# Kernel tuning notes

Hardware: AMD Instinct MI355X
Metric: run time of the kernel (lower is better)

Reference implementation:

```python
import jax, jax.numpy as jnp
import numpy as np

N_NODES = 50000
N_EDGES = 800000
NODE_DIM = 256
EDGE_DIM = 64
NUM_REL = 4
HID = 512      # hidden_dims[0]
LAST = 128     # last_dim_size
BATCH = 16384
EPS = 1e-10    # torchdrug RelationalGraphConv degree-normalization eps


def _glorot(k, shape):
    fan_in = shape[-1]
    return jax.random.normal(k, shape, jnp.float32) / np.sqrt(fan_in).astype(np.float32)


def setup_inputs() -> dict:
    key = jax.random.key(0)
    ks = jax.random.split(key, 20)
    inp = {}
    inp["inputs"] = jax.random.randint(ks[0], (BATCH, 3), 0, N_NODES, dtype=jnp.int32)
    inp["node_feature"] = jax.random.normal(ks[1], (N_NODES, NODE_DIM), jnp.float32)
    inp["edge_feature"] = jax.random.normal(ks[2], (N_EDGES, EDGE_DIM), jnp.float32)
    inp["edge_src"] = jax.random.randint(ks[3], (N_EDGES,), 0, N_NODES, dtype=jnp.int32)
    inp["edge_dst"] = jax.random.randint(ks[4], (N_EDGES,), 0, N_NODES, dtype=jnp.int32)
    inp["edge_rel"] = jax.random.randint(ks[5], (N_EDGES,), 0, NUM_REL, dtype=jnp.int32)
    # RGCN layer 1: 256 -> 512
    inp["We1"] = _glorot(ks[6], (NODE_DIM, EDGE_DIM)); inp["be1"] = jnp.zeros((NODE_DIM,), jnp.float32)
    inp["Wl1"] = _glorot(ks[7], (HID, NUM_REL * NODE_DIM)); inp["bl1"] = jnp.zeros((HID,), jnp.float32)
    inp["Ws1"] = _glorot(ks[8], (HID, NODE_DIM)); inp["bs1"] = jnp.zeros((HID,), jnp.float32)
    # RGCN layer 2: 512 -> 128
    inp["We2"] = _glorot(ks[9], (HID, EDGE_DIM)); inp["be2"] = jnp.zeros((HID,), jnp.float32)
    inp["Wl2"] = _glorot(ks[10], (LAST, NUM_REL * HID)); inp["bl2"] = jnp.zeros((LAST,), jnp.float32)
    inp["Ws2"] = _glorot(ks[11], (LAST, HID)); inp["bs2"] = jnp.zeros((LAST,), jnp.float32)
    # ccle_mlp: edge_dim -> 256 -> 128
    inp["Wc1"] = _glorot(ks[12], (256, EDGE_DIM)); inp["bc1"] = jnp.zeros((256,), jnp.float32)
    inp["Wc2"] = _glorot(ks[13], (LAST, 256)); inp["bc2"] = jnp.zeros((LAST,), jnp.float32)
    # final MLP: 3*128 -> 128 -> 64 -> 1
    inp["Wf1"] = _glorot(ks[14], (128, 3 * LAST)); inp["bf1"] = jnp.zeros((128,), jnp.float32)
    inp["Wf2"] = _glorot(ks[15], (64, 128)); inp["bf2"] = jnp.zeros((64,), jnp.float32)
    inp["Wf3"] = _glorot(ks[16], (1, 64)); inp["bf3"] = jnp.zeros((1,), jnp.float32)
    return inp


def _rgcn_layer(x, edge_src, edge_dst, edge_rel, edge_feat, We, be, Wl, bl, Ws, bs):
    """torchdrug RelationalGraphConv: message = x[src] + edge_linear(edge_feat);
    per-(node,relation) mean aggregation; combine = linear(update) + self_loop(x); relu."""
    in_dim = x.shape[1]
    msg = x[edge_src] + edge_feat @ We.T + be                      # [E, in_dim]
    seg = edge_dst * NUM_REL + edge_rel                            # [E]
    agg = jax.ops.segment_sum(msg, seg, num_segments=N_NODES * NUM_REL)
    cnt = jax.ops.segment_sum(jnp.ones((msg.shape[0], 1), msg.dtype), seg,
                              num_segments=N_NODES * NUM_REL)
    upd = (agg / (cnt + EPS)).reshape(N_NODES, NUM_REL * in_dim)   # [N, R*in_dim]
    return jax.nn.relu(upd @ Wl.T + bl + x @ Ws.T + bs)


def reference(inputs, node_feature, edge_feature, edge_src, edge_dst, edge_rel,
              We1, be1, Wl1, bl1, Ws1, bs1,
              We2, be2, Wl2, bl2, Ws2, bs2,
              Wc1, bc1, Wc2, bc2,
              Wf1, bf1, Wf2, bf2, Wf3, bf3):
    d1, d2, ctx = inputs[:, 0], inputs[:, 1], inputs[:, 2]
    h = _rgcn_layer(node_feature, edge_src, edge_dst, edge_rel, edge_feature,
                    We1, be1, Wl1, bl1, Ws1, bs1)
    h = _rgcn_layer(h, edge_src, edge_dst, edge_rel, edge_feature,
                    We2, be2, Wl2, bl2, Ws2, bs2)
    x1 = h[d1]                                                     # [B, 128]
    x2 = h[d2]                                                     # [B, 128]
    ef = edge_feature[ctx]                                         # [B, 64]
    x3 = jax.nn.relu(ef @ Wc1.T + bc1) @ Wc2.T + bc2               # [B, 128]
    x = jnp.concatenate([x1, x2, x3], axis=1)                      # [B, 384]
    x = jax.nn.relu(x @ Wf1.T + bf1)
    x = jax.nn.relu(x @ Wf2.T + bf2)
    return x @ Wf3.T + bf3                                         # [B, 1]
```

## Files before the change

kernel.cpp:

```cpp
#include <hip/hip_runtime.h>
#include <hip/hip_bf16.h>

#define N_NODES 50000
#define N_EDGES 800000
#define NODE_DIM 256
#define EDGE_DIM 64
#define NUM_REL 4
#define HID 512
#define LAST 128
#define BATCH 16384
#define EPS 1e-10f
#define NSEG (N_NODES * NUM_REL)

#define K1 1600
#define K2 832

typedef __bf16 bf16_t;
typedef __attribute__((ext_vector_type(8))) __bf16 bf16x8;
typedef __attribute__((ext_vector_type(4))) __bf16 bf16x4;
typedef __attribute__((ext_vector_type(2))) __bf16 bf16x2;
typedef __attribute__((ext_vector_type(4))) float f32x4;

typedef __attribute__((address_space(1))) const unsigned int g_u32;
typedef __attribute__((address_space(3))) unsigned int l_u32;
static __device__ __forceinline__ void gload16(const void* g, void* l) {
    __builtin_amdgcn_global_load_lds((g_u32*)g, (l_u32*)l, 16, 0, 0);
}

__global__ __launch_bounds__(256) void hist_kernel(
    const int* __restrict__ edst, const int* __restrict__ erel, int* __restrict__ hist)
{
    int e = blockIdx.x * 256 + threadIdx.x;
    if (e >= N_EDGES) return;
    atomicAdd(&hist[edst[e] * NUM_REL + erel[e]], 1);
}

#define SCAN_B 2048
__global__ __launch_bounds__(256) void scan1(
    const int* __restrict__ in, int* __restrict__ out, int* __restrict__ bsum, int n)
{
    __shared__ int sh[256];
    int base = blockIdx.x * SCAN_B + threadIdx.x * 8;
    int v[8]; int s = 0;
#pragma unroll
    for (int i = 0; i < 8; ++i) {
        int idx = base + i;
        v[i] = s;
        s += (idx < n) ? in[idx] : 0;
    }
    sh[threadIdx.x] = s;
    __syncthreads();
    for (int off = 1; off < 256; off <<= 1) {
        int t = (threadIdx.x >= off) ? sh[threadIdx.x - off] : 0;
        __syncthreads();
        sh[threadIdx.x] += t;
        __syncthreads();
    }
    int texcl = (threadIdx.x == 0) ? 0 : sh[threadIdx.x - 1];
#pragma unroll
    for (int i = 0; i < 8; ++i) {
        int idx = base + i;
        if (idx < n) out[idx] = texcl + v[i];
    }
    if (threadIdx.x == 255) bsum[blockIdx.x] = sh[255];
}

__global__ void scan2(int* bsum, int nb)
{
    if (threadIdx.x == 0 && blockIdx.x == 0) {
        int s = 0;
        for (int i = 0; i < nb; ++i) { int t = bsum[i]; bsum[i] = s; s += t; }
    }
}

__global__ __launch_bounds__(256) void scan3(int* __restrict__ out, const int* __restrict__ bsum, int n)
{
    int idx = blockIdx.x * SCAN_B + threadIdx.x * 8;
    int add = bsum[blockIdx.x];
#pragma unroll
    for (int i = 0; i < 8; ++i)
        if (idx + i < n) out[idx + i] += add;
}

__global__ __launch_bounds__(256) void csr_fill(
    const int* __restrict__ edst, const int* __restrict__ erel, const int* __restrict__ esrc,
    const int* __restrict__ offs, int* __restrict__ cursor,
    int* __restrict__ csr_src, int* __restrict__ csr_eid)
{
    int e = blockIdx.x * 256 + threadIdx.x;
    if (e >= N_EDGES) return;
    int seg = edst[e] * NUM_REL + erel[e];
    int pos = offs[seg] + atomicAdd(&cursor[seg], 1);
    csr_src[pos] = esrc[e];
    csr_eid[pos] = e;
}

__global__ __launch_bounds__(256) void prep_small(
    const float* __restrict__ Wc1, const float* __restrict__ Wc2,
    const float* __restrict__ Wf1, const float* __restrict__ Wf2,
    const float* __restrict__ bl1, const float* __restrict__ bs1,
    const float* __restrict__ bl2, const float* __restrict__ bs2,
    bf16_t* __restrict__ Wc1b, bf16_t* __restrict__ Wc2b,
    bf16_t* __restrict__ Wf1b, bf16_t* __restrict__ Wf2b,
    float* __restrict__ bias12, float* __restrict__ bias22)
{
    int i = blockIdx.x * 256 + threadIdx.x;
    const float* src; bf16_t* dst; int base;
    if (i < 4096)        { src = Wc1; dst = Wc1b; base = 0; }
    else if (i < 12288)  { src = Wc2; dst = Wc2b; base = 4096; }
    else if (i < 24576)  { src = Wf1; dst = Wf1b; base = 12288; }
    else if (i < 26624)  { src = Wf2; dst = Wf2b; base = 24576; }
    else {
        int j = i - 26624;
        if (j < 512) bias12[j] = bl1[j] + bs1[j];
        else if (j < 640) bias22[j - 512] = bl2[j - 512] + bs2[j - 512];
        return;
    }
    int k = i - base;
    float4 v = ((const float4*)src)[k];
    bf16x4 o;
    o[0] = (bf16_t)v.x; o[1] = (bf16_t)v.y; o[2] = (bf16_t)v.z; o[3] = (bf16_t)v.w;
    ((bf16x4*)dst)[k] = o;
}

__global__ __launch_bounds__(256) void xconv_k(const float* __restrict__ x, bf16_t* __restrict__ A1,
                                               bf16_t* __restrict__ xb)
{
    int i = blockIdx.x * 256 + threadIdx.x;
    int n = i >> 6;
    int c4 = i & 63;
    float4 v = ((const float4*)(x + (size_t)n * 256))[c4];
    bf16x4 o;
    o[0] = (bf16_t)v.x; o[1] = (bf16_t)v.y; o[2] = (bf16_t)v.z; o[3] = (bf16_t)v.w;
    *(bf16x4*)(A1 + (size_t)n * K1 + 1280 + c4 * 4) = o;
    *(bf16x4*)(xb + (size_t)n * 256 + c4 * 4) = o;
}

__global__ __launch_bounds__(256) void prep_w1cat(
    const float* __restrict__ Wl1, const float* __restrict__ We1,
    const float* __restrict__ Ws1, const float* __restrict__ be1, bf16_t* __restrict__ W1cat)
{
    int j = blockIdx.x;
    int t = threadIdx.x;
    const float* wrow = Wl1 + (size_t)j * 1024;
    bf16_t* out = W1cat + (size_t)j * K1;
    for (int c = t; c < 1024; c += 256) out[c] = (bf16_t)wrow[c];
    {
        int r = t >> 6, e = t & 63;
        float s = 0.f;
        const float* wr = wrow + r * 256;
        for (int c = 0; c < 256; ++c) s += wr[c] * We1[c * 64 + e];
        out[1024 + t] = (bf16_t)s;
    }
    if (t < 256) out[1280 + t] = (bf16_t)Ws1[(size_t)j * 256 + t];
    if (t < 4) {
        float s = 0.f;
        const float* wr = wrow + t * 256;
        for (int c = 0; c < 256; ++c) s += wr[c] * be1[c];
        out[1536 + t] = (bf16_t)s;
    }
    if (t >= 4 && t < 64) out[1536 + t] = (bf16_t)0.f;
}

__global__ __launch_bounds__(256) void prep_w2cat(
    const float* __restrict__ Wl2, const float* __restrict__ We2,
    const float* __restrict__ Ws2, const float* __restrict__ be2, bf16_t* __restrict__ W2cat)
{
    int j = blockIdx.x;
    int t = threadIdx.x;
    const float* wrow = Wl2 + (size_t)j * 2048;
    bf16_t* out = W2cat + (size_t)j * K2;
    {
        int r = t >> 6, e = t & 63;
        float s = 0.f;
        const float* wr = wrow + r * 512;
        for (int k = 0; k < 512; ++k) s += wr[k] * We2[k * 64 + e];
        out[t] = (bf16_t)s;
    }
    for (int c = t; c < 512; c += 256) out[256 + c] = (bf16_t)Ws2[(size_t)j * 512 + c];
    if (t < 4) {
        float s = 0.f;
        const float* wr = wrow + t * 512;
        for (int k = 0; k < 512; ++k) s += wr[k] * be2[k];
        out[768 + t] = (bf16_t)s;
    }
    if (t >= 4 && t < 64) out[768 + t] = (bf16_t)0.f;
}

__global__ __launch_bounds__(256) void prep_w2p(const float* __restrict__ Wl2, bf16_t* __restrict__ W2p)
{
    int idx = blockIdx.x * 256 + threadIdx.x;
    int row = idx >> 9, k = idx & 511;
    int j = row & 127, r = row >> 7;
    W2p[idx] = (bf16_t)Wl2[(size_t)j * 2048 + r * 512 + k];
}

__global__ __launch_bounds__(256) void agg1(
    const float* __restrict__ ef, const bf16_t* __restrict__ xb,
    const int* __restrict__ csr_src, const int* __restrict__ csr_eid,
    const int* __restrict__ offs, const int* __restrict__ hist,
    bf16_t* __restrict__ A1, bf16_t* __restrict__ A2)
{
    int n = blockIdx.x;
    int w = threadIdx.x >> 6;
    int lane = threadIdx.x & 63;
    int half = lane >> 5;
    int l32 = lane & 31;
    int seg = n * NUM_REL + w;
    int beg = offs[seg], ct = hist[seg];

    float xs[8] = {0.f, 0.f, 0.f, 0.f, 0.f, 0.f, 0.f, 0.f};
    float es0 = 0.f, es1 = 0.f;

    int i = 0;
    for (; i + 4 <= ct; i += 4) {
        int sA = csr_src[beg + i + half];
        int sB = csr_src[beg + i + 2 + half];
        int eA = csr_eid[beg + i + half];
        int eB = csr_eid[beg + i + 2 + half];
        bf16x8 vA = *(const bf16x8*)(xb + (size_t)sA * 256 + l32 * 8);
        bf16x8 vB = *(const bf16x8*)(xb + (size_t)sB * 256 + l32 * 8);
        float2 fA = *(const float2*)(ef + (size_t)eA * 64 + l32 * 2);
        float2 fB = *(const float2*)(ef + (size_t)eB * 64 + l32 * 2);
#pragma unroll
        for (int j = 0; j < 8; ++j) xs[j] += (float)vA[j] + (float)vB[j];
        es0 += fA.x + fB.x;
        es1 += fA.y + fB.y;
    }
    for (; i + 2 <= ct; i += 2) {
        int sA = csr_src[beg + i + half];
        int eA = csr_eid[beg + i + half];
        bf16x8 vA = *(const bf16x8*)(xb + (size_t)sA * 256 + l32 * 8);
        float2 fA = *(const float2*)(ef + (size_t)eA * 64 + l32 * 2);
#pragma unroll
        for (int j = 0; j < 8; ++j) xs[j] += (float)vA[j];
        es0 += fA.x;
        es1 += fA.y;
    }
    if (i < ct && half == 0) {
        int sA = csr_src[beg + i];
        int eA = csr_eid[beg + i];
        bf16x8 vA = *(const bf16x8*)(xb + (size_t)sA * 256 + l32 * 8);
        float2 fA = *(const float2*)(ef + (size_t)eA * 64 + l32 * 2);
#pragma unroll
        for (int j = 0; j < 8; ++j) xs[j] += (float)vA[j];
        es0 += fA.x;
        es1 += fA.y;
    }
#pragma unroll
    for (int j = 0; j < 8; ++j) xs[j] += __shfl_xor(xs[j], 32);
    es0 += __shfl_xor(es0, 32);
    es1 += __shfl_xor(es1, 32);

    float inv = 1.0f / ((float)ct + EPS);
    if (half == 0) {
        bf16x8 m;
#pragma unroll
        for (int j = 0; j < 8; ++j) m[j] = (bf16_t)(xs[j] * inv);
        *(bf16x8*)(A1 + (size_t)n * K1 + w * 256 + l32 * 8) = m;
        bf16x2 e2;
        e2[0] = (bf16_t)(es0 * inv);
        e2[1] = (bf16_t)(es1 * inv);
        *(bf16x2*)(A1 + (size_t)n * K1 + 1024 + w * 64 + l32 * 2) = e2;
        *(bf16x2*)(A2 + (size_t)n * K2 + w * 64 + l32 * 2) = e2;
    }
    if (lane == 0) {
        bf16_t fv = (bf16_t)((float)ct * inv);
        A1[(size_t)n * K1 + 1536 + w] = fv;
        A2[(size_t)n * K2 + 768 + w] = fv;
    }
    if (w == 3 && lane >= 4) {
        A1[(size_t)n * K1 + 1536 + lane] = (bf16_t)0.f;
        A2[(size_t)n * K2 + 768 + lane] = (bf16_t)0.f;
    }
}

__global__ __launch_bounds__(256) void agg2(
    const bf16_t* __restrict__ P, const int* __restrict__ csr_src,
    const int* __restrict__ offs, const int* __restrict__ hist,
    float* __restrict__ h2base)
{
    __shared__ float red[4][128];
    int n = blockIdx.x;
    int w = threadIdx.x >> 6;
    int lane = threadIdx.x & 63;
    int half = lane >> 5;
    int l32 = lane & 31;
    int seg = n * NUM_REL + w;
    int beg = offs[seg], ct = hist[seg];

    float s0 = 0.f, s1 = 0.f, s2 = 0.f, s3 = 0.f;
    int i = 0;
    for (; i + 4 <= ct; i += 4) {
        int a = csr_src[beg + i + half];
        int b = csr_src[beg + i + 2 + half];
        bf16x4 va = *(const bf16x4*)(P + (size_t)a * HID + w * 128 + l32 * 4);
        bf16x4 vb = *(const bf16x4*)(P + (size_t)b * HID + w * 128 + l32 * 4);
        s0 += (float)va[0] + (float)vb[0];
        s1 += (float)va[1] + (float)vb[1];
        s2 += (float)va[2] + (float)vb[2];
        s3 += (float)va[3] + (float)vb[3];
    }
    for (; i + 2 <= ct; i += 2) {
        int a = csr_src[beg + i + half];
        bf16x4 va = *(const bf16x4*)(P + (size_t)a * HID + w * 128 + l32 * 4);
        s0 += (float)va[0]; s1 += (float)va[1]; s2 += (float)va[2]; s3 += (float)va[3];
    }
    if (i < ct && half == 0) {
        int a = csr_src[beg + i];
        bf16x4 va = *(const bf16x4*)(P + (size_t)a * HID + w * 128 + l32 * 4);
        s0 += (float)va[0]; s1 += (float)va[1]; s2 += (float)va[2]; s3 += (float)va[3];
    }
    s0 += __shfl_xor(s0, 32);
    s1 += __shfl_xor(s1, 32);
    s2 += __shfl_xor(s2, 32);
    s3 += __shfl_xor(s3, 32);

    float inv = 1.0f / ((float)ct + EPS);
    if (half == 0) {
        red[w][l32 * 4 + 0] = s0 * inv;
        red[w][l32 * 4 + 1] = s1 * inv;
        red[w][l32 * 4 + 2] = s2 * inv;
        red[w][l32 * 4 + 3] = s3 * inv;
    }
    __syncthreads();
    int t = threadIdx.x;
    if (t < 128)
        h2base[(size_t)n * 128 + t] = red[0][t] + red[1][t] + red[2][t] + red[3][t];
}

template<int RELU, int ACC, int OUTBF>
__global__ __launch_bounds__(256) void gemm_bf16(
    const bf16_t* __restrict__ A, int lda,
    const bf16_t* __restrict__ W, int ldw,
    const float* __restrict__ Cin, int ldcin,
    const float* __restrict__ bias,
    void* __restrict__ Cout, int ldc,
    int M, int N, int K, int ncol)
{
    __shared__ char smem[32768];
    char* As = smem;
    char* Bs = smem + 16384;
    const int tid = threadIdx.x;
    const int row0 = (blockIdx.x / ncol) * 128;
    const int col0 = (blockIdx.x % ncol) * 128;
    const int lane = tid & 63, wv = tid >> 6;

    const int rsub = lane >> 3;
    const int gchunk = (lane & 7) ^ rsub;
    const bf16_t* pa[4]; const bf16_t* pb[4];
    char* la[4]; char* lb[4];
#pragma unroll
    for (int s = 0; s < 4; ++s) {
        int q = wv * 4 + s;
        int ar = row0 + q * 8 + rsub; if (ar >= M) ar = M - 1;
        int br = col0 + q * 8 + rsub; if (br >= N) br = N - 1;
        pa[s] = A + (size_t)ar * lda + gchunk * 8;
        pb[s] = W + (size_t)br * ldw + gchunk * 8;
        la[s] = As + q * 1024;
        lb[s] = Bs + q * 1024;
    }

    const int wm = wv >> 1, wn = wv & 1;
    const int r16 = lane & 15, kch = lane >> 4;
    const int sw = r16 & 7;

    f32x4 zero = {0.f, 0.f, 0.f, 0.f};
    f32x4 acc[4][4];
#pragma unroll
    for (int i = 0; i < 4; ++i)
#pragma unroll
        for (int j = 0; j < 4; ++j) acc[i][j] = zero;

    for (int k0 = 0; k0 < K; k0 += 64) {
#pragma unroll
        for (int s = 0; s < 4; ++s) {
            gload16(pa[s] + k0, la[s]);
            gload16(pb[s] + k0, lb[s]);
        }
        __syncthreads();
#pragma unroll
        for (int t = 0; t < 2; ++t) {
            const int slot = ((t * 4 + kch) ^ sw) << 4;
            bf16x8 af[4], bfm[4];
#pragma unroll
            for (int i = 0; i < 4; ++i)
                af[i] = *(const bf16x8*)(As + (wm * 64 + i * 16 + r16) * 128 + slot);
#pragma unroll
            for (int j = 0; j < 4; ++j)
                bfm[j] = *(const bf16x8*)(Bs + (wn * 64 + j * 16 + r16) * 128 + slot);
#pragma unroll
            for (int i = 0; i < 4; ++i)
#pragma unroll
                for (int j = 0; j < 4; ++j)
                    acc[i][j] = __builtin_amdgcn_mfma_f32_16x16x32_bf16(af[i], bfm[j], acc[i][j], 0, 0, 0);
        }
        __syncthreads();
    }

    const int crow0 = row0 + wm * 64;
#pragma unroll
    for (int i = 0; i < 4; ++i) {
#pragma unroll
        for (int j = 0; j < 4; ++j) {
            int col = col0 + wn * 64 + j * 16 + r16;
            if (col >= N) continue;
            float bv = bias ? bias[col] : 0.f;
#pragma unroll
            for (int q = 0; q < 4; ++q) {
                int row = crow0 + i * 16 + kch * 4 + q;
                if (row >= M) continue;
                float v = acc[i][j][q] + bv;
                if (ACC) v += Cin[(size_t)row * ldcin + col];
                if (RELU) v = fmaxf(v, 0.f);
                if (OUTBF) ((bf16_t*)Cout)[(size_t)row * ldc + col] = (bf16_t)v;
                else       ((float*)Cout)[(size_t)row * ldc + col] = v;
            }
        }
    }
}

__global__ __launch_bounds__(256) void gather_head(
    const int* __restrict__ inputs, const bf16_t* __restrict__ h2,
    const float* __restrict__ ef, bf16_t* __restrict__ xcat, bf16_t* __restrict__ ef_g)
{
    int i = blockIdx.x;
    int t = threadIdx.x;
    int d1 = inputs[i * 3 + 0];
    int d2 = inputs[i * 3 + 1];
    int ctx = inputs[i * 3 + 2];
    if (t < 128) {
        xcat[(size_t)i * 384 + t] = h2[(size_t)d1 * LAST + t];
    } else {
        int c = t - 128;
        xcat[(size_t)i * 384 + 128 + c] = h2[(size_t)d2 * LAST + c];
    }
    if (t < 64) ef_g[(size_t)i * 64 + t] = (bf16_t)ef[(size_t)ctx * EDGE_DIM + t];
}

__global__ __launch_bounds__(256) void final_matvec(
    const bf16_t* __restrict__ f2, const float* __restrict__ Wf3,
    const float* __restrict__ bf3, float* __restrict__ out, int M)
{
    int row = blockIdx.x * 4 + (threadIdx.x >> 6);
    int lane = threadIdx.x & 63;
    if (row >= M) return;
    float v = (float)f2[(size_t)row * 64 + lane] * Wf3[lane];
#pragma unroll
    for (int off = 32; off > 0; off >>= 1) v += __shfl_down(v, off);
    if (lane == 0) out[row] = v + bf3[0];
}

extern "C" void kernel_launch(void* const* d_in, const int* in_sizes, int n_in,
                              void* d_out, int out_size, void* d_ws, size_t ws_size,
                              hipStream_t stream)
{
    const int*   inputs       = (const int*)  d_in[0];
    const float* node_feature = (const float*)d_in[1];
    const float* edge_feature = (const float*)d_in[2];
    const int*   edge_src     = (const int*)  d_in[3];
    const int*   edge_dst     = (const int*)  d_in[4];
    const int*   edge_rel     = (const int*)  d_in[5];
    const float* We1 = (const float*)d_in[6];
    const float* be1 = (const float*)d_in[7];
    const float* Wl1 = (const float*)d_in[8];
    const float* bl1 = (const float*)d_in[9];
    const float* Ws1 = (const float*)d_in[10];
    const float* bs1 = (const float*)d_in[11];
    const float* We2 = (const float*)d_in[12];
    const float* be2 = (const float*)d_in[13];
    const float* Wl2 = (const float*)d_in[14];
    const float* bl2 = (const float*)d_in[15];
    const float* Ws2 = (const float*)d_in[16];
    const float* bs2 = (const float*)d_in[17];
    const float* Wc1 = (const float*)d_in[18];
    const float* bc1 = (const float*)d_in[19];
    const float* Wc2 = (const float*)d_in[20];
    const float* bc2 = (const float*)d_in[21];
    const float* Wf1 = (const float*)d_in[22];
    const float* bf1 = (const float*)d_in[23];
    const float* Wf2 = (const float*)d_in[24];
    const float* bf2 = (const float*)d_in[25];
    const float* Wf3 = (const float*)d_in[26];
    const float* bf3 = (const float*)d_in[27];
    float* out = (float*)d_out;

    char* p = (char*)d_ws;
    auto alloc = [&](size_t bytes) { char* r = p; p += (bytes + 255) & ~(size_t)255; return r; };
    int* hist     = (int*)alloc(NSEG * 4);
    int* offs     = (int*)alloc(NSEG * 4);
    int* cursor   = (int*)alloc(NSEG * 4);
    int* csr_src  = (int*)alloc(N_EDGES * 4);
    int* csr_eid  = (int*)alloc(N_EDGES * 4);
    int* bsums    = (int*)alloc(128 * 4);
    bf16_t* A1    = (bf16_t*)alloc((size_t)N_NODES * K1 * 2);
    bf16_t* A2    = (bf16_t*)alloc((size_t)N_NODES * K2 * 2);
    bf16_t* xb    = (bf16_t*)alloc((size_t)N_NODES * 256 * 2);
    bf16_t* Pbuf  = (bf16_t*)alloc((size_t)N_NODES * HID * 2);
    float*  h2base= (float*)alloc((size_t)N_NODES * 128 * 4);
    bf16_t* h2    = (bf16_t*)alloc((size_t)N_NODES * 128 * 2);
    bf16_t* W1cat = (bf16_t*)alloc((size_t)512 * K1 * 2);
    bf16_t* W2cat = (bf16_t*)alloc((size_t)128 * K2 * 2);
    bf16_t* W2p   = (bf16_t*)alloc((size_t)512 * 512 * 2);
    bf16_t* Wc1b  = (bf16_t*)alloc(256 * 64 * 2);
    bf16_t* Wc2b  = (bf16_t*)alloc(128 * 256 * 2);
    bf16_t* Wf1b  = (bf16_t*)alloc(128 * 384 * 2);
    bf16_t* Wf2b  = (bf16_t*)alloc(64 * 128 * 2);
    float*  bias12= (float*)alloc(512 * 4);
    float*  bias22= (float*)alloc(128 * 4);
    bf16_t* ef_g  = (bf16_t*)alloc((size_t)BATCH * 64 * 2);
    bf16_t* u3    = (bf16_t*)alloc((size_t)BATCH * 256 * 2);
    bf16_t* xcat  = (bf16_t*)alloc((size_t)BATCH * 384 * 2);
    bf16_t* f1    = (bf16_t*)alloc((size_t)BATCH * 128 * 2);
    bf16_t* f2    = (bf16_t*)alloc((size_t)BATCH * 64 * 2);

    hipMemsetAsync(hist, 0, NSEG * 4, stream);
    hipMemsetAsync(cursor, 0, NSEG * 4, stream);
    hist_kernel<<<(N_EDGES + 255) / 256, 256, 0, stream>>>(edge_dst, edge_rel, hist);
    int nscan = (NSEG + SCAN_B - 1) / SCAN_B;
    scan1<<<nscan, 256, 0, stream>>>(hist, offs, bsums, NSEG);
    scan2<<<1, 64, 0, stream>>>(bsums, nscan);
    scan3<<<nscan, 256, 0, stream>>>(offs, bsums, NSEG);
    csr_fill<<<(N_EDGES + 255) / 256, 256, 0, stream>>>(edge_dst, edge_rel, edge_src,
                                                        offs, cursor, csr_src, csr_eid);

    prep_w1cat<<<512, 256, 0, stream>>>(Wl1, We1, Ws1, be1, W1cat);
    prep_w2cat<<<128, 256, 0, stream>>>(Wl2, We2, Ws2, be2, W2cat);
    prep_w2p<<<(512 * 512) / 256, 256, 0, stream>>>(Wl2, W2p);
    prep_small<<<(26624 + 640 + 255) / 256, 256, 0, stream>>>(
        Wc1, Wc2, Wf1, Wf2, bl1, bs1, bl2, bs2,
        Wc1b, Wc2b, Wf1b, Wf2b, bias12, bias22);
    xconv_k<<<(N_NODES * 64 + 255) / 256, 256, 0, stream>>>(node_feature, A1, xb);

    agg1<<<N_NODES, 256, 0, stream>>>(edge_feature, xb, csr_src, csr_eid, offs, hist, A1, A2);
    {
        int nrow = (N_NODES + 127) / 128, ncol = HID / 128;
        gemm_bf16<1, 0, 1><<<nrow * ncol, 256, 0, stream>>>(A1, K1, W1cat, K1, nullptr, 0, bias12,
                                                            A2 + 256, K2, N_NODES, HID, K1, ncol);
    }

    {
        int nrow = (N_NODES + 127) / 128, ncol = HID / 128;
        gemm_bf16<0, 0, 1><<<nrow * ncol, 256, 0, stream>>>(A2 + 256, K2, W2p, 512, nullptr, 0, nullptr,
                                                            Pbuf, HID, N_NODES, HID, 512, ncol);
    }
    agg2<<<N_NODES, 256, 0, stream>>>(Pbuf, csr_src, offs, hist, h2base);
    {
        int nrow = (N_NODES + 127) / 128;
        gemm_bf16<1, 1, 1><<<nrow, 256, 0, stream>>>(A2, K2, W2cat, K2, h2base, 128, bias22,
                                                     h2, 128, N_NODES, 128, K2, 1);
    }

    gather_head<<<BATCH, 256, 0, stream>>>(inputs, h2, edge_feature, xcat, ef_g);
    {
        gemm_bf16<1, 0, 1><<<(BATCH / 128) * 2, 256, 0, stream>>>(ef_g, 64, Wc1b, 64, nullptr, 0, bc1,
                                                                  u3, 256, BATCH, 256, 64, 2);
    }
    {
        gemm_bf16<0, 0, 1><<<BATCH / 128, 256, 0, stream>>>(u3, 256, Wc2b, 256, nullptr, 0, bc2,
                                                            xcat + 256, 384, BATCH, 128, 256, 1);
    }
    {
        gemm_bf16<1, 0, 1><<<BATCH / 128, 256, 0, stream>>>(xcat, 384, Wf1b, 384, nullptr, 0, bf1,
                                                            f1, 128, BATCH, 128, 384, 1);
    }
    {
        gemm_bf16<1, 0, 1><<<BATCH / 128, 256, 0, stream>>>(f1, 128, Wf2b, 128, nullptr, 0, bf2,
                                                            f2, 64, BATCH, 64, 128, 1);
    }
    final_matvec<<<BATCH / 4, 256, 0, stream>>>(f2, Wf3, bf3, out, BATCH);
}
```

Measured before the change: 730.6 us.

## Double-buffer A tiles in LDS and load W fragments directly from global

The GEMM kernel now stages only A tiles in LDS, using the full 32KB as a double buffer so the next K-slice's A load is issued before the current slice's MFMAs run. This removes one of the two barriers per iteration. W fragments are read straight from global memory into registers per wave and rely on cache reuse, since the weights are small. The risk is higher global/L2 traffic and latency exposure for the W reads, which are no longer shared through LDS across the two waves that use them.

```diff
diff --git a/kernel.cpp b/kernel.cpp
--- a/kernel.cpp
+++ b/kernel.cpp
@@ -339,8 +339,6 @@
     int M, int N, int K, int ncol)
 {
     __shared__ char smem[32768];
-    char* As = smem;
-    char* Bs = smem + 16384;
     const int tid = threadIdx.x;
     const int row0 = (blockIdx.x / ncol) * 128;
     const int col0 = (blockIdx.x % ncol) * 128;
@@ -348,47 +346,56 @@
 
     const int rsub = lane >> 3;
     const int gchunk = (lane & 7) ^ rsub;
-    const bf16_t* pa[4]; const bf16_t* pb[4];
-    char* la[4]; char* lb[4];
+    const bf16_t* pa[4];
+    int lao[4];
 #pragma unroll
     for (int s = 0; s < 4; ++s) {
         int q = wv * 4 + s;
         int ar = row0 + q * 8 + rsub; if (ar >= M) ar = M - 1;
-        int br = col0 + q * 8 + rsub; if (br >= N) br = N - 1;
         pa[s] = A + (size_t)ar * lda + gchunk * 8;
-        pb[s] = W + (size_t)br * ldw + gchunk * 8;
-        la[s] = As + q * 1024;
-        lb[s] = Bs + q * 1024;
+        lao[s] = q * 1024;
     }
 
     const int wm = wv >> 1, wn = wv & 1;
     const int r16 = lane & 15, kch = lane >> 4;
     const int sw = r16 & 7;
 
-    f32x4 zero = {0.f, 0.f, 0.f, 0.f};
+    const bf16_t* pw[4];
+#pragma unroll
+    for (int j = 0; j < 4; ++j) {
+        int br = col0 + wn * 64 + j * 16 + r16; if (br >= N) br = N - 1;
+        pw[j] = W + (size_t)br * ldw + kch * 8;
+    }
+
     f32x4 acc[4][4];
 #pragma unroll
     for (int i = 0; i < 4; ++i)
 #pragma unroll
-        for (int j = 0; j < 4; ++j) acc[i][j] = zero;
-
+        for (int j = 0; j < 4; ++j) acc[i][j] = (f32x4){0.f, 0.f, 0.f, 0.f};
+
+#pragma unroll
+    for (int s = 0; s < 4; ++s) gload16(pa[s], smem + lao[s]);
+    __syncthreads();
+
+    int cur = 0;
     for (int k0 = 0; k0 < K; k0 += 64) {
-#pragma unroll
-        for (int s = 0; s < 4; ++s) {
-            gload16(pa[s] + k0, la[s]);
-            gload16(pb[s] + k0, lb[s]);
+        if (k0 + 64 < K) {
+#pragma unroll
+            for (int s = 0; s < 4; ++s)
+                gload16(pa[s] + k0 + 64, smem + ((cur ^ 1) << 14) + lao[s]);
         }
-        __syncthreads();
+        const char* As = smem + (cur << 14);
 #pragma unroll
         for (int t = 0; t < 2; ++t) {
+            bf16x8 bfm[4];
+#pragma unroll
+            for (int j = 0; j < 4; ++j)
+                bfm[j] = *(const bf16x8*)(pw[j] + k0 + t * 32);
             const int slot = ((t * 4 + kch) ^ sw) << 4;
-            bf16x8 af[4], bfm[4];
+            bf16x8 af[4];
 #pragma unroll
             for (int i = 0; i < 4; ++i)
                 af[i] = *(const bf16x8*)(As + (wm * 64 + i * 16 + r16) * 128 + slot);
-#pragma unroll
-            for (int j = 0; j < 4; ++j)
-                bfm[j] = *(const bf16x8*)(Bs + (wn * 64 + j * 16 + r16) * 128 + slot);
 #pragma unroll
             for (int i = 0; i < 4; ++i)
 #pragma unroll
@@ -396,6 +403,7 @@
                     acc[i][j] = __builtin_amdgcn_mfma_f32_16x16x32_bf16(af[i], bfm[j], acc[i][j], 0, 0, 0);
         }
         __syncthreads();
+        cur ^= 1;
     }
 
     const int crow0 = row0 + wm * 64;
```

Measured after the change: 850.9 us. 1.16x slower.
